# Kernel optimization log

Measured on AMD Instinct MI355X. Metric: run time of the kernel, lower is better.

Reference implementation:

```python
import jax, jax.numpy as jnp
import numpy as np

N = 50000   # nodes
E = 600000  # edges
F = 128     # num_features (= in_channels = out_channels of EvolveGCNO)
C = 2       # num_classes


def setup_inputs() -> dict:
    key = jax.random.key(0)
    ks = jax.random.split(key, 8)
    s = 1.0 / np.sqrt(F)
    x = jax.random.normal(ks[0], (N, F), jnp.float32)
    edge_index = jax.random.randint(ks[1], (2, E), 0, N, jnp.int64)
    W0 = jax.random.uniform(ks[2], (F, F), jnp.float32, -s, s)      # initial GCN weight (glorot-ish)
    w_ih = jax.random.uniform(ks[3], (4 * F, F), jnp.float32, -s, s)  # LSTM input-hidden
    w_hh = jax.random.uniform(ks[4], (4 * F, F), jnp.float32, -s, s)  # LSTM hidden-hidden
    b_ih = jax.random.uniform(ks[5], (4 * F,), jnp.float32, -s, s)
    b_hh = jax.random.uniform(ks[6], (4 * F,), jnp.float32, -s, s)
    gcn_bias = jnp.zeros((F,), jnp.float32)
    Wc = jax.random.uniform(ks[7], (C, F), jnp.float32, -s, s)       # classifier nn.Linear(F, C)
    bc = jnp.zeros((C,), jnp.float32)
    return dict(x=x, W0=W0, w_ih=w_ih, w_hh=w_hh, b_ih=b_ih, b_hh=b_hh,
                gcn_bias=gcn_bias, Wc=Wc, bc=bc, edge_index=edge_index)


def reference(x, W0, w_ih, w_hh, b_ih, b_hh, gcn_bias, Wc, bc, edge_index):
    n = x.shape[0]
    # --- EvolveGCN-O weight evolution: one LSTM step on the FxF weight,
    # rows of W0 are the LSTM "batch", initial hidden/cell state are zero.
    gates = W0 @ w_ih.T + b_ih + b_hh            # [F, 4F]  (h=0 so w_hh term vanishes)
    i, f, g, o = jnp.split(gates, 4, axis=1)     # PyTorch gate order: i, f, g, o
    c = jax.nn.sigmoid(i) * jnp.tanh(g)          # c0 = 0 -> f-gate term drops
    W = jax.nn.sigmoid(o) * jnp.tanh(c)          # evolved GCN weight [F, F]

    # --- GCN normalization with self-loops: D^-1/2 (A + I) D^-1/2
    loop = jnp.arange(n, dtype=edge_index.dtype)
    row = jnp.concatenate([edge_index[0], loop])  # source
    col = jnp.concatenate([edge_index[1], loop])  # target
    ew = jnp.ones(row.shape[0], x.dtype)
    deg = jax.ops.segment_sum(ew, col, num_segments=n)
    dis = jnp.where(deg > 0, jax.lax.rsqrt(jnp.maximum(deg, 1.0)), 0.0)
    norm = dis[row] * dis[col]                    # [E+N]

    # --- GCNConv_Fixed_W: transform then aggregate messages at targets
    xw = x @ W                                    # [N, F]
    msg = norm[:, None] * xw[row]                 # gather + scale
    h = jax.ops.segment_sum(msg, col, num_segments=n) + gcn_bias  # scatter-add

    h = jax.nn.relu(h)
    # dropout(p=0.3) is identity in eval mode
    return h @ Wc.T + bc                          # [N, C]
```

## Files before the change

### kernel.cpp

```cpp
#include <hip/hip_runtime.h>
#include <hip/hip_bf16.h>

#define F 128
#define CAP 32
#define NF 1024

typedef __bf16 bf16x8 __attribute__((ext_vector_type(8)));
typedef float f32x4 __attribute__((ext_vector_type(4)));

static __device__ __forceinline__ unsigned int f2bfbits(float f) {
  unsigned int u = __float_as_uint(f);
  return (u + 0x7fffu + ((u >> 16) & 1u)) >> 16;
}

__global__ __launch_bounds__(256) void lstm_zero_kernel(
    const float* __restrict__ W0, const float* __restrict__ w_ih,
    const float* __restrict__ b_ih, const float* __restrict__ b_hh,
    unsigned short* __restrict__ Wt, int* __restrict__ deg,
    int* __restrict__ ovf_cnt, int n) {
  __shared__ __align__(16) float srow[4][F];
  __shared__ float sg[4][4 * F];
  int b = blockIdx.x, t = threadIdx.x;
  if (b < 32) {
    int r0 = b * 4;
    for (int i = t; i < 4 * F; i += 256)
      srow[i >> 7][i & 127] = W0[(size_t)(r0 + (i >> 7)) * F + (i & 127)];
    __syncthreads();
#pragma unroll
    for (int half = 0; half < 2; half++) {
      int gc = t + half * 256;
      float acc[4] = {0.f, 0.f, 0.f, 0.f};
      const float4* wv4 = (const float4*)(w_ih + (size_t)gc * F);
#pragma unroll 4
      for (int k4 = 0; k4 < F / 4; k4++) {
        float4 w = wv4[k4];
#pragma unroll
        for (int i = 0; i < 4; i++) {
          float4 s = *(const float4*)&srow[i][k4 * 4];
          acc[i] = fmaf(s.x, w.x, fmaf(s.y, w.y, fmaf(s.z, w.z, fmaf(s.w, w.w, acc[i]))));
        }
      }
      float bias = b_ih[gc] + b_hh[gc];
#pragma unroll
      for (int i = 0; i < 4; i++) sg[i][gc] = acc[i] + bias;
    }
    __syncthreads();
#pragma unroll
    for (int half = 0; half < 2; half++) {
      int idx2 = t + half * 256;
      int rr = idx2 >> 7, c = idx2 & 127;
      float gi = sg[rr][c], gg = sg[rr][c + 2 * F], go = sg[rr][c + 3 * F];
      float si = 1.f / (1.f + expf(-gi));
      float so = 1.f / (1.f + expf(-go));
      float cc2 = si * tanhf(gg);
      Wt[(size_t)c * F + r0 + rr] = (unsigned short)f2bfbits(so * tanhf(cc2));
    }
  } else {
    int stride = ((int)gridDim.x - 32) * 256;
    for (int i = (b - 32) * 256 + t; i < n; i += stride) deg[i] = 0;
    if (b == 32 && t == 0) *ovf_cnt = 0;
  }
}

__global__ __launch_bounds__(256) void fill_xw_kernel(
    const int* __restrict__ row, const int* __restrict__ col,
    int* __restrict__ deg, unsigned short* __restrict__ bucket,
    int* __restrict__ ovf_cnt, int* __restrict__ ovf,
    const float* __restrict__ x, const unsigned short* __restrict__ Wt,
    unsigned short* __restrict__ xwb, int n, int e) {
  int b = blockIdx.x, t = threadIdx.x;
  if (b < NF) {
    int g = b & 7;
    int cg = b >> 3;
    const int stride = (NF / 8) * 256;
    for (int i = cg * 256 + t; i < e; i += stride) {
      int c = col[i];
      if ((c & 7) == g) {
        int r = row[i];
        int p = atomicAdd(&deg[c], 1);
        if (p < CAP) {
          bucket[(size_t)c * CAP + p] = (unsigned short)r;
        } else {
          int q = atomicAdd(ovf_cnt, 1);
          ovf[2 * q + 0] = c;
          ovf[2 * q + 1] = r;
        }
      }
    }
  } else {
    int w = t >> 6, l = t & 63;
    int q = l >> 4, m = l & 15;
    int m0 = (b - NF) * 64 + w * 16;
    int arow = m0 + m;
    bf16x8 a[4];
    const float4* xr4 = (const float4*)(x + (size_t)arow * F);
    bool rv = arow < n;
#pragma unroll
    for (int kc = 0; kc < 4; kc++) {
      uint4 pk = make_uint4(0u, 0u, 0u, 0u);
      if (rv) {
        float4 v0 = xr4[kc * 8 + q * 2 + 0];
        float4 v1 = xr4[kc * 8 + q * 2 + 1];
        pk.x = f2bfbits(v0.x) | (f2bfbits(v0.y) << 16);
        pk.y = f2bfbits(v0.z) | (f2bfbits(v0.w) << 16);
        pk.z = f2bfbits(v1.x) | (f2bfbits(v1.y) << 16);
        pk.w = f2bfbits(v1.z) | (f2bfbits(v1.w) << 16);
      }
      a[kc] = __builtin_bit_cast(bf16x8, pk);
    }
#pragma unroll
    for (int nc = 0; nc < 8; nc++) {
      f32x4 acc = {0.f, 0.f, 0.f, 0.f};
#pragma unroll
      for (int kc = 0; kc < 4; kc++) {
        uint4 bu = *(const uint4*)(Wt + (size_t)(nc * 16 + m) * F + kc * 32 + q * 8);
        acc = __builtin_amdgcn_mfma_f32_16x16x32_bf16(
            a[kc], __builtin_bit_cast(bf16x8, bu), acc, 0, 0, 0);
      }
#pragma unroll
      for (int r = 0; r < 4; r++) {
        int gr = m0 + q * 4 + r;
        if (gr < n)
          xwb[(size_t)gr * F + nc * 16 + m] = (unsigned short)f2bfbits(acc[r]);
      }
    }
  }
}

__global__ __launch_bounds__(256) void agg_kernel(
    const int* __restrict__ deg, const unsigned short* __restrict__ bucket,
    const unsigned int* __restrict__ xwb, const int* __restrict__ ovf_cnt,
    const int* __restrict__ ovf, const float* __restrict__ gcn_bias,
    const float* __restrict__ Wc, const float* __restrict__ bc,
    float* __restrict__ out, int n) {
  int wave = threadIdx.x >> 6;
  int lane = threadIdx.x & 63;
  int v = blockIdx.x * 4 + wave;
  if (v >= n) return;
  int d = deg[v];
  float dv = rsqrtf((float)(d + 1));
  float ax, ay;
  {
    unsigned int u = xwb[(size_t)v * 64 + lane];
    float sl = dv * dv;
    ax = sl * __uint_as_float(u << 16);
    ay = sl * __uint_as_float(u & 0xffff0000u);
  }
  int eend = d < CAP ? d : CAP;
  const unsigned short* bkt = bucket + (size_t)v * CAP;
  if (eend > 0) {
    int s[16];
    float nr[16];
    unsigned int u[16];
#pragma unroll
    for (int q = 0; q < 16; q++) s[q] = bkt[q < eend ? q : 0];
#pragma unroll
    for (int q = 0; q < 16; q++) {
      float msk = (q < eend) ? 1.f : 0.f;
      nr[q] = rsqrtf((float)(deg[s[q]] + 1)) * dv * msk;
    }
#pragma unroll
    for (int q = 0; q < 16; q++) u[q] = xwb[(size_t)s[q] * 64 + lane];
#pragma unroll
    for (int q = 0; q < 16; q++) {
      ax = fmaf(nr[q], __uint_as_float(u[q] << 16), ax);
      ay = fmaf(nr[q], __uint_as_float(u[q] & 0xffff0000u), ay);
    }
    for (int j = 16; j < eend; j += 8) {
      int s2[8];
      float nr2[8];
      unsigned int u2[8];
#pragma unroll
      for (int q = 0; q < 8; q++) s2[q] = bkt[j + q < eend ? j + q : 0];
#pragma unroll
      for (int q = 0; q < 8; q++) {
        float msk = (j + q < eend) ? 1.f : 0.f;
        nr2[q] = rsqrtf((float)(deg[s2[q]] + 1)) * dv * msk;
      }
#pragma unroll
      for (int q = 0; q < 8; q++) u2[q] = xwb[(size_t)s2[q] * 64 + lane];
#pragma unroll
      for (int q = 0; q < 8; q++) {
        ax = fmaf(nr2[q], __uint_as_float(u2[q] << 16), ax);
        ay = fmaf(nr2[q], __uint_as_float(u2[q] & 0xffff0000u), ay);
      }
    }
  }
  if (d > CAP) {
    int oc = *ovf_cnt;
    for (int k = 0; k < oc; k++) {
      if (ovf[2 * k] == v) {
        int s = ovf[2 * k + 1];
        float nrr = rsqrtf((float)(deg[s] + 1)) * dv;
        unsigned int u = xwb[(size_t)s * 64 + lane];
        ax = fmaf(nrr, __uint_as_float(u << 16), ax);
        ay = fmaf(nrr, __uint_as_float(u & 0xffff0000u), ay);
      }
    }
  }
  int f0 = lane * 2;
  float h0 = fmaxf(ax + gcn_bias[f0], 0.f);
  float h1 = fmaxf(ay + gcn_bias[f0 + 1], 0.f);
  float a0 = h0 * Wc[f0] + h1 * Wc[f0 + 1];
  float a1 = h0 * Wc[F + f0] + h1 * Wc[F + f0 + 1];
#pragma unroll
  for (int off = 32; off > 0; off >>= 1) {
    a0 += __shfl_down(a0, off);
    a1 += __shfl_down(a1, off);
  }
  if (lane == 0) {
    out[(size_t)v * 2 + 0] = a0 + bc[0];
    out[(size_t)v * 2 + 1] = a1 + bc[1];
  }
}

extern "C" void kernel_launch(void* const* d_in, const int* in_sizes, int n_in,
                              void* d_out, int out_size, void* d_ws, size_t ws_size,
                              hipStream_t stream) {
  const float* x        = (const float*)d_in[0];
  const float* W0       = (const float*)d_in[1];
  const float* w_ih     = (const float*)d_in[2];
  const float* b_ih     = (const float*)d_in[4];
  const float* b_hh     = (const float*)d_in[5];
  const float* gcn_bias = (const float*)d_in[6];
  const float* Wc       = (const float*)d_in[7];
  const float* bc       = (const float*)d_in[8];
  const int*   ei       = (const int*)d_in[9];

  const int n = in_sizes[0] / F;
  const int e = in_sizes[9] / 2;
  const int* row = ei;
  const int* col = ei + e;

  char* wsb = (char*)d_ws;
  unsigned short* Wt = (unsigned short*)wsb;  wsb += 32768;
  size_t n4 = ((size_t)n * 4 + 255) & ~(size_t)255;
  int*   deg     = (int*)wsb;                 wsb += n4;
  int*   ovf_cnt = deg + n;
  int*   ovf     = (int*)wsb;                 wsb += 8192;
  unsigned short* bucket = (unsigned short*)wsb;
  wsb += (size_t)n * CAP * 2;
  unsigned short* xwb = (unsigned short*)wsb;

  const int NT = (n + 63) / 64;

  lstm_zero_kernel<<<32 + 128, 256, 0, stream>>>(W0, w_ih, b_ih, b_hh, Wt,
                                                 deg, ovf_cnt, n);

  fill_xw_kernel<<<NF + NT, 256, 0, stream>>>(row, col, deg, bucket, ovf_cnt,
                                              ovf, x, Wt, xwb, n, e);

  agg_kernel<<<(n + 3) / 4, 256, 0, stream>>>(deg, bucket,
                                              (const unsigned int*)xwb,
                                              ovf_cnt, ovf, gcn_bias, Wc, bc,
                                              (float*)d_out, n);
}
```

Baseline: 163.4 us.

## Prescale xw by source degree into fp16 and pad degree counters per cacheline

Adds a pass that multiplies each node's xw row by its own rsqrt degree and stores it as fp16, so aggregation no longer gathers per-edge source degrees and applies the target scale once at the end. Degree counters are padded to one per 64 bytes to cut atomic contention and false sharing, bucket indices are loaded as two vector loads, and the overflow list is bounded. The costs are an extra kernel launch with a full read-write pass over xw, a degree array sixteen times larger, and a switch from bf16 to fp16 storage that changes precision and range.

```diff
diff --git a/kernel.cpp b/kernel.cpp
--- a/kernel.cpp
+++ b/kernel.cpp
@@ -1,9 +1,11 @@
 #include <hip/hip_runtime.h>
 #include <hip/hip_bf16.h>
+#include <hip/hip_fp16.h>
 
 #define F 128
 #define CAP 32
 #define NF 1024
+#define OVF_MAX 1024
 
 typedef __bf16 bf16x8 __attribute__((ext_vector_type(8)));
 typedef float f32x4 __attribute__((ext_vector_type(4)));
@@ -12,6 +14,7 @@
   unsigned int u = __float_as_uint(f);
   return (u + 0x7fffu + ((u >> 16) & 1u)) >> 16;
 }
+
 
 __global__ __launch_bounds__(256) void lstm_zero_kernel(
     const float* __restrict__ W0, const float* __restrict__ w_ih,
@@ -57,7 +60,10 @@
     }
   } else {
     int stride = ((int)gridDim.x - 32) * 256;
-    for (int i = (b - 32) * 256 + t; i < n; i += stride) deg[i] = 0;
+    int4* dz = (int4*)deg;
+    int total4 = n * 4;
+    const int4 z = make_int4(0, 0, 0, 0);
+    for (int i = (b - 32) * 256 + t; i < total4; i += stride) dz[i] = z;
     if (b == 32 && t == 0) *ovf_cnt = 0;
   }
 }
@@ -77,13 +83,15 @@
       int c = col[i];
       if ((c & 7) == g) {
         int r = row[i];
-        int p = atomicAdd(&deg[c], 1);
+        int p = atomicAdd(&deg[(size_t)c * 16], 1);
         if (p < CAP) {
           bucket[(size_t)c * CAP + p] = (unsigned short)r;
         } else {
           int q = atomicAdd(ovf_cnt, 1);
-          ovf[2 * q + 0] = c;
-          ovf[2 * q + 1] = r;
+          if (q < OVF_MAX) {
+            ovf[2 * q + 0] = c;
+            ovf[2 * q + 1] = r;
+          }
         }
       }
     }
@@ -127,9 +135,28 @@
   }
 }
 
+__global__ __launch_bounds__(256) void scale_kernel(
+    const int* __restrict__ deg, unsigned short* __restrict__ xwb, int n) {
+  int i = blockIdx.x * 256 + threadIdx.x;
+  if (i >= n * 16) return;
+  int v = i >> 4;
+  float dv = rsqrtf((float)(deg[(size_t)v * 16] + 1));
+  uint4 u = ((uint4*)xwb)[i];
+  unsigned int w[4] = {u.x, u.y, u.z, u.w};
+#pragma unroll
+  for (int k = 0; k < 4; k++) {
+    float lo = __uint_as_float(w[k] << 16) * dv;
+    float hi = __uint_as_float(w[k] & 0xffff0000u) * dv;
+    unsigned short hl = __half_as_ushort(__float2half_rn(lo));
+    unsigned short hh = __half_as_ushort(__float2half_rn(hi));
+    w[k] = (unsigned int)hl | ((unsigned int)hh << 16);
+  }
+  ((uint4*)xwb)[i] = make_uint4(w[0], w[1], w[2], w[3]);
+}
+
 __global__ __launch_bounds__(256) void agg_kernel(
     const int* __restrict__ deg, const unsigned short* __restrict__ bucket,
-    const unsigned int* __restrict__ xwb, const int* __restrict__ ovf_cnt,
+    const unsigned int* __restrict__ ywb, const int* __restrict__ ovf_cnt,
     const int* __restrict__ ovf, const float* __restrict__ gcn_bias,
     const float* __restrict__ Wc, const float* __restrict__ bc,
     float* __restrict__ out, int n) {
@@ -137,70 +164,65 @@
   int lane = threadIdx.x & 63;
   int v = blockIdx.x * 4 + wave;
   if (v >= n) return;
-  int d = deg[v];
+  int d = deg[(size_t)v * 16];
   float dv = rsqrtf((float)(d + 1));
   float ax, ay;
   {
-    unsigned int u = xwb[(size_t)v * 64 + lane];
-    float sl = dv * dv;
-    ax = sl * __uint_as_float(u << 16);
-    ay = sl * __uint_as_float(u & 0xffff0000u);
+    unsigned int u = ywb[(size_t)v * 64 + lane];
+    ax = __half2float(__ushort_as_half((unsigned short)(u & 0xffffu)));
+    ay = __half2float(__ushort_as_half((unsigned short)(u >> 16)));
   }
   int eend = d < CAP ? d : CAP;
   const unsigned short* bkt = bucket + (size_t)v * CAP;
   if (eend > 0) {
+    uint4 b0 = *(const uint4*)(bkt);
+    uint4 b1 = *(const uint4*)(bkt + 8);
+    unsigned int wv[8] = {b0.x, b0.y, b0.z, b0.w, b1.x, b1.y, b1.z, b1.w};
     int s[16];
-    float nr[16];
     unsigned int u[16];
 #pragma unroll
-    for (int q = 0; q < 16; q++) s[q] = bkt[q < eend ? q : 0];
+    for (int q = 0; q < 16; q++) {
+      int raw = (q & 1) ? (int)(wv[q >> 1] >> 16) : (int)(wv[q >> 1] & 0xffffu);
+      s[q] = (q < eend) ? raw : 0;
+    }
+#pragma unroll
+    for (int q = 0; q < 16; q++) u[q] = ywb[(size_t)s[q] * 64 + lane];
 #pragma unroll
     for (int q = 0; q < 16; q++) {
       float msk = (q < eend) ? 1.f : 0.f;
-      nr[q] = rsqrtf((float)(deg[s[q]] + 1)) * dv * msk;
-    }
-#pragma unroll
-    for (int q = 0; q < 16; q++) u[q] = xwb[(size_t)s[q] * 64 + lane];
-#pragma unroll
-    for (int q = 0; q < 16; q++) {
-      ax = fmaf(nr[q], __uint_as_float(u[q] << 16), ax);
-      ay = fmaf(nr[q], __uint_as_float(u[q] & 0xffff0000u), ay);
+      ax = fmaf(msk, __half2float(__ushort_as_half((unsigned short)(u[q] & 0xffffu))), ax);
+      ay = fmaf(msk, __half2float(__ushort_as_half((unsigned short)(u[q] >> 16))), ay);
     }
     for (int j = 16; j < eend; j += 8) {
       int s2[8];
-      float nr2[8];
       unsigned int u2[8];
 #pragma unroll
       for (int q = 0; q < 8; q++) s2[q] = bkt[j + q < eend ? j + q : 0];
+#pragma unroll
+      for (int q = 0; q < 8; q++) u2[q] = ywb[(size_t)s2[q] * 64 + lane];
 #pragma unroll
       for (int q = 0; q < 8; q++) {
         float msk = (j + q < eend) ? 1.f : 0.f;
-        nr2[q] = rsqrtf((float)(deg[s2[q]] + 1)) * dv * msk;
-      }
-#pragma unroll
-      for (int q = 0; q < 8; q++) u2[q] = xwb[(size_t)s2[q] * 64 + lane];
-#pragma unroll
-      for (int q = 0; q < 8; q++) {
-        ax = fmaf(nr2[q], __uint_as_float(u2[q] << 16), ax);
-        ay = fmaf(nr2[q], __uint_as_float(u2[q] & 0xffff0000u), ay);
+        ax = fmaf(msk, __half2float(__ushort_as_half((unsigned short)(u2[q] & 0xffffu))), ax);
+        ay = fmaf(msk, __half2float(__ushort_as_half((unsigned short)(u2[q] >> 16))), ay);
       }
     }
   }
   if (d > CAP) {
     int oc = *ovf_cnt;
+    if (oc > OVF_MAX) oc = OVF_MAX;
     for (int k = 0; k < oc; k++) {
       if (ovf[2 * k] == v) {
-        int s = ovf[2 * k + 1];
-        float nrr = rsqrtf((float)(deg[s] + 1)) * dv;
-        unsigned int u = xwb[(size_t)s * 64 + lane];
-        ax = fmaf(nrr, __uint_as_float(u << 16), ax);
-        ay = fmaf(nrr, __uint_as_float(u & 0xffff0000u), ay);
+        int s3 = ovf[2 * k + 1];
+        unsigned int uu = ywb[(size_t)s3 * 64 + lane];
+        ax += __half2float(__ushort_as_half((unsigned short)(uu & 0xffffu)));
+        ay += __half2float(__ushort_as_half((unsigned short)(uu >> 16)));
       }
     }
   }
   int f0 = lane * 2;
-  float h0 = fmaxf(ax + gcn_bias[f0], 0.f);
-  float h1 = fmaxf(ay + gcn_bias[f0 + 1], 0.f);
+  float h0 = fmaxf(fmaf(dv, ax, gcn_bias[f0]), 0.f);
+  float h1 = fmaxf(fmaf(dv, ay, gcn_bias[f0 + 1]), 0.f);
   float a0 = h0 * Wc[f0] + h1 * Wc[f0 + 1];
   float a1 = h0 * Wc[F + f0] + h1 * Wc[F + f0 + 1];
 #pragma unroll
@@ -234,10 +256,9 @@
 
   char* wsb = (char*)d_ws;
   unsigned short* Wt = (unsigned short*)wsb;  wsb += 32768;
-  size_t n4 = ((size_t)n * 4 + 255) & ~(size_t)255;
-  int*   deg     = (int*)wsb;                 wsb += n4;
-  int*   ovf_cnt = deg + n;
-  int*   ovf     = (int*)wsb;                 wsb += 8192;
+  int*   deg     = (int*)wsb;                 wsb += (size_t)n * 64;
+  int*   ovf_cnt = (int*)wsb;                 wsb += 256;
+  int*   ovf     = (int*)wsb;                 wsb += 8 * OVF_MAX;
   unsigned short* bucket = (unsigned short*)wsb;
   wsb += (size_t)n * CAP * 2;
   unsigned short* xwb = (unsigned short*)wsb;
@@ -249,6 +270,8 @@
 
   fill_xw_kernel<<<NF + NT, 256, 0, stream>>>(row, col, deg, bucket, ovf_cnt,
                                               ovf, x, Wt, xwb, n, e);
+
+  scale_kernel<<<(n * 16 + 255) / 256, 256, 0, stream>>>(deg, xwb, n);
 
   agg_kernel<<<(n + 3) / 4, 256, 0, stream>>>(deg, bucket,
                                               (const unsigned int*)xwb,
```

After: 157.9 us. 1.03x faster.
